# Optimization experiments

Hardware: AMD Instinct MI355X
Metric: run time of the kernel (lower is better)

## Reference

```python
import jax, jax.numpy as jnp
import numpy as np

# B=batch, T=time, H=hidden_size, D=vocos_dim, I=intermediate_dim, L=num_layers,
# CB=codebook_size, CD=codebook_dim (factorized VQ)
B, T, H, D, I, L, CB, CD = 8, 2048, 1024, 384, 2048, 12, 8192, 8


def _ln(h, g, b, eps=1e-6):
    # torch LayerNorm over last dim (biased variance)
    m = h.mean(-1, keepdims=True)
    v = h.var(-1, keepdims=True)
    return (h - m) / jnp.sqrt(v + eps) * g + b


def _conv1d(x, w, b, groups=1):
    # x: (B, Cin, T), w: (Cout, Cin//groups, 7), same-pad k=7
    y = jax.lax.conv_general_dilated(
        x, w, window_strides=(1,), padding=[(3, 3)],
        dimension_numbers=('NCH', 'OIH', 'NCH'), feature_group_count=groups)
    return y + b[None, :, None]


def setup_inputs() -> dict:
    key = jax.random.key(0)
    ks = iter(jax.random.split(key, 32))
    def nrm(shape):
        return jax.random.normal(next(ks), shape, jnp.float32) * 0.02
    d = {}
    d['x'] = jax.random.normal(next(ks), (B, T, H), jnp.float32)
    # VocosBackbone (encoder): embed conv + LN + 12 ConvNeXt blocks + final LN
    d['enc_embed_w'] = nrm((D, H, 7)); d['enc_embed_b'] = jnp.zeros((D,), jnp.float32)
    d['enc_norm_g'] = jnp.ones((D,), jnp.float32); d['enc_norm_b'] = jnp.zeros((D,), jnp.float32)
    d['enc_dw_w'] = nrm((L, D, 1, 7)); d['enc_dw_b'] = jnp.zeros((L, D), jnp.float32)
    d['enc_ln_g'] = jnp.ones((L, D), jnp.float32); d['enc_ln_b'] = jnp.zeros((L, D), jnp.float32)
    d['enc_w1'] = nrm((L, I, D)); d['enc_b1'] = jnp.zeros((L, I), jnp.float32)
    d['enc_w2'] = nrm((L, D, I)); d['enc_b2'] = jnp.zeros((L, D), jnp.float32)
    d['enc_gamma'] = jnp.full((L, D), 1.0 / L, jnp.float32)  # layer_scale init 1/num_layers
    d['enc_fnorm_g'] = jnp.ones((D,), jnp.float32); d['enc_fnorm_b'] = jnp.zeros((D,), jnp.float32)
    # nn.Linear(vocos_dim, hidden_size)
    d['enc_out_w'] = nrm((H, D)); d['enc_out_b'] = jnp.zeros((H,), jnp.float32)
    # Factorized ResidualVQ (single quantizer): 1024 -> 8, 8192-entry codebook, 8 -> 1024
    d['vq_in_w'] = nrm((CD, H)); d['vq_in_b'] = jnp.zeros((CD,), jnp.float32)
    d['codebook'] = jax.random.normal(next(ks), (CB, CD), jnp.float32)
    d['vq_out_w'] = nrm((H, CD)); d['vq_out_b'] = jnp.zeros((H,), jnp.float32)
    return d


def _encode(x, ew, eb, ng, nb, dww, dwb, lng, lnb, w1, b1, w2, b2, gamma, fg, fb, ow, ob):
    # x: (B, T, H) -> encoder output (B, T, H)
    h = _conv1d(x.transpose(0, 2, 1), ew, eb)            # (B, D, T)
    h = _ln(h.transpose(0, 2, 1), ng, nb)                # (B, T, D)
    for i in range(L):
        res = h
        y = _conv1d(h.transpose(0, 2, 1), dww[i], dwb[i], groups=D)  # depthwise (B, D, T)
        y = _ln(y.transpose(0, 2, 1), lng[i], lnb[i])                # (B, T, D)
        y = jax.nn.gelu(y @ w1[i].T + b1[i], approximate=False)       # (B, T, I)
        y = (y @ w2[i].T + b2[i]) * gamma[i]                          # (B, T, D)
        h = res + y
    h = _ln(h, fg, fb)
    return h @ ow.T + ob                                  # (B, T, H)


def _quantize(enc, in_w, in_b, codebook, out_w, out_b):
    z_e = enc @ in_w.T + in_b                             # (B, T, CD)
    z_n = z_e / jnp.maximum(jnp.linalg.norm(z_e, axis=-1, keepdims=True), 1e-12)
    cb_n = codebook / jnp.maximum(jnp.linalg.norm(codebook, axis=-1, keepdims=True), 1e-12)
    sim = jnp.einsum('btd,nd->btn', z_n, cb_n)            # cosine sim == argmin l2 on normalized vecs
    idx = jnp.argmax(sim, axis=-1)                        # (B, T) int
    z_q = codebook[idx]                                   # (B, T, CD) unnormalized codebook entries
    z_q = z_e + jax.lax.stop_gradient(z_q - z_e)          # straight-through estimator
    quantized = z_q @ out_w.T + out_b                     # (B, T, H)
    return idx, quantized


def reference(x, enc_embed_w, enc_embed_b, enc_norm_g, enc_norm_b, enc_dw_w, enc_dw_b,
              enc_ln_g, enc_ln_b, enc_w1, enc_b1, enc_w2, enc_b2, enc_gamma,
              enc_fnorm_g, enc_fnorm_b, enc_out_w, enc_out_b,
              vq_in_w, vq_in_b, codebook, vq_out_w, vq_out_b):
    enc = _encode(x, enc_embed_w, enc_embed_b, enc_norm_g, enc_norm_b, enc_dw_w, enc_dw_b,
                  enc_ln_g, enc_ln_b, enc_w1, enc_b1, enc_w2, enc_b2, enc_gamma,
                  enc_fnorm_g, enc_fnorm_b, enc_out_w, enc_out_b)
    idx, quantized = _quantize(enc, vq_in_w, vq_in_b, codebook, vq_out_w, vq_out_b)
    # RepCodec.quantize returns (indices (B,T), quantized_out.transpose(1,2) -> (B,T,H))
    return idx, quantized
```

## Files before the change

### kernel.cpp

```cpp
#include <hip/hip_runtime.h>
#include <math.h>


typedef _Float16 h8_t __attribute__((ext_vector_type(8)));
typedef _Float16 h4_t __attribute__((ext_vector_type(4)));
typedef float f4_t __attribute__((ext_vector_type(4)));

__device__ __forceinline__ float gelu_exact(float x){
  return 0.5f * x * (1.0f + erff(x * 0.70710678118654752f));
}

__device__ __forceinline__ void split8(const float4& a, const float4& b, h8_t& hi, h8_t& lo){
  float f[8] = {a.x,a.y,a.z,a.w,b.x,b.y,b.z,b.w};
  #pragma unroll
  for (int t=0;t<8;t++){
    _Float16 hh = (_Float16)f[t];
    hi[t] = hh;
    lo[t] = (_Float16)(f[t] - (float)hh);
  }
}

__device__ __forceinline__ void split4(const float4& a, h4_t& hi, h4_t& lo){
  float f[4] = {a.x,a.y,a.z,a.w};
  #pragma unroll
  for (int t=0;t<4;t++){
    _Float16 hh = (_Float16)f[t];
    hi[t] = hh;
    lo[t] = (_Float16)(f[t] - (float)hh);
  }
}

__device__ __forceinline__ int swz(int row, int kg){
  return row*32 + ((kg ^ ((row>>1)&3))<<3);
}

__device__ __forceinline__ void xcd_remap(int& bx, int& by){
  const int gx = gridDim.x;
  const int nwg = gx * gridDim.y;
  int bid = by*gx + bx;
  if ((nwg & 7) == 0){
    bid = (bid & 7)*(nwg >> 3) + (bid >> 3);
    bx = bid % gx; by = bid / gx;
  }
}


__global__ __launch_bounds__(256) void prep_wk_split(const float* __restrict__ w,
                                                     _Float16* __restrict__ wh,
                                                     _Float16* __restrict__ wl){
  int i = blockIdx.x*256 + threadIdx.x;
  if (i >= 384*1024) return;
  int d = i >> 10, c = i & 1023;
  #pragma unroll
  for (int k=0;k<7;k++){
    float v = w[(size_t)d*(1024*7) + (size_t)c*7 + k];
    _Float16 hh = (_Float16)v;
    wh[(size_t)k*393216 + i] = hh;
    wl[(size_t)k*393216 + i] = (_Float16)(v - (float)hh);
  }
}

__global__ __launch_bounds__(256) void prep_cb(const float* __restrict__ cb, float* __restrict__ cbn){
  int e = blockIdx.x*256 + threadIdx.x;
  if (e >= 8192) return;
  float v[8], s = 0.f;
  #pragma unroll
  for (int cd=0; cd<8; ++cd){ v[cd] = cb[(size_t)e*8+cd]; s += v[cd]*v[cd]; }
  float inv = 1.0f / fmaxf(sqrtf(s), 1e-12f);
  #pragma unroll
  for (int cd=0; cd<8; ++cd) cbn[(size_t)e*8+cd] = v[cd]*inv;
}

__global__ __launch_bounds__(256) void split_pair(const float* __restrict__ a, const float* __restrict__ b,
                                                  _Float16* __restrict__ ah, _Float16* __restrict__ al,
                                                  _Float16* __restrict__ bh, _Float16* __restrict__ bl,
                                                  int n4){
  int i = blockIdx.x*256 + threadIdx.x;
  if (i >= n4) return;
  h4_t hi, lo;
  float4 va = ((const float4*)a)[i];
  split4(va, hi, lo);
  ((h4_t*)ah)[i] = hi; ((h4_t*)al)[i] = lo;
  float4 vb = ((const float4*)b)[i];
  split4(vb, hi, lo);
  ((h4_t*)bh)[i] = hi; ((h4_t*)bl)[i] = lo;
}

__global__ __launch_bounds__(256) void split_one(const float* __restrict__ a,
                                                 _Float16* __restrict__ ah, _Float16* __restrict__ al,
                                                 int n4){
  int i = blockIdx.x*256 + threadIdx.x;
  if (i >= n4) return;
  h4_t hi, lo;
  float4 va = ((const float4*)a)[i];
  split4(va, hi, lo);
  ((h4_t*)ah)[i] = hi; ((h4_t*)al)[i] = lo;
}

template<int BN, int EPI>
__global__ __launch_bounds__(256,2) void gemm_s(
    const _Float16* __restrict__ Ah, const _Float16* __restrict__ Al, int lda,
    const _Float16* __restrict__ Bh, const _Float16* __restrict__ Bl, int ldb,
    const float* __restrict__ bias, const float* __restrict__ gamma,
    float* __restrict__ C, _Float16* __restrict__ Ch, _Float16* __restrict__ Cl,
    int ldc, int K)
{
  constexpr int NF = BN/32;
  __shared__ _Float16 AsH[4096], AsL[4096];
  __shared__ _Float16 BsH[BN*32], BsL[BN*32];
  const int tid = threadIdx.x;
  int bx = blockIdx.x, by = blockIdx.y;
  xcd_remap(bx, by);
  const int m0 = by*128, n0 = bx*BN;
  const int srow = tid>>2, kgs = tid&3, koff = kgs*8;
  const _Float16* pAh = Ah + (size_t)(m0+srow)*lda + koff;
  const _Float16* pAl = Al + (size_t)(m0+srow)*lda + koff;
  const _Float16* pBh = Bh + (size_t)(n0+srow)*ldb + koff;
  const _Float16* pBl = Bl + (size_t)(n0+srow)*ldb + koff;
  const int sA0 = swz(srow, kgs), sA1 = swz(srow+64, kgs);
  const int lane = tid & 63, wid = tid >> 6;
  const int wm = (wid>>1)*64, wn = (wid&1)*(BN/2);
  const int fr = lane & 15, kg = lane >> 4;
  f4_t acc[4][NF] = {};
  h8_t rah0 = *(const h8_t*)(pAh);
  h8_t rah1 = *(const h8_t*)(pAh + (size_t)64*lda);
  h8_t ral0 = *(const h8_t*)(pAl);
  h8_t ral1 = *(const h8_t*)(pAl + (size_t)64*lda);
  h8_t rbh0 = *(const h8_t*)(pBh);
  h8_t rbl0 = *(const h8_t*)(pBl);
  h8_t rbh1, rbl1;
  if constexpr (BN == 128){
    rbh1 = *(const h8_t*)(pBh + (size_t)64*ldb);
    rbl1 = *(const h8_t*)(pBl + (size_t)64*ldb);
  }
  for (int k0 = 0; k0 < K; k0 += 32){
    __syncthreads();
    *(h8_t*)(AsH + sA0) = rah0; *(h8_t*)(AsL + sA0) = ral0;
    *(h8_t*)(AsH + sA1) = rah1; *(h8_t*)(AsL + sA1) = ral1;
    *(h8_t*)(BsH + sA0) = rbh0; *(h8_t*)(BsL + sA0) = rbl0;
    if constexpr (BN == 128){
      *(h8_t*)(BsH + sA1) = rbh1; *(h8_t*)(BsL + sA1) = rbl1;
    }
    if (k0 + 32 < K){
      const int kn = k0 + 32;
      rah0 = *(const h8_t*)(pAh + kn);
      rah1 = *(const h8_t*)(pAh + (size_t)64*lda + kn);
      ral0 = *(const h8_t*)(pAl + kn);
      ral1 = *(const h8_t*)(pAl + (size_t)64*lda + kn);
      rbh0 = *(const h8_t*)(pBh + kn);
      rbl0 = *(const h8_t*)(pBl + kn);
      if constexpr (BN == 128){
        rbh1 = *(const h8_t*)(pBh + (size_t)64*ldb + kn);
        rbl1 = *(const h8_t*)(pBl + (size_t)64*ldb + kn);
      }
    }
    __syncthreads();
    h8_t ah[4], al[4], bh[NF], bl[NF];
    #pragma unroll
    for (int m=0;m<4;m++){
      int o = swz(wm + fr + m*16, kg);
      ah[m] = *(const h8_t*)(AsH + o);
      al[m] = *(const h8_t*)(AsL + o);
    }
    #pragma unroll
    for (int n=0;n<NF;n++){
      int o = swz(wn + fr + n*16, kg);
      bh[n] = *(const h8_t*)(BsH + o);
      bl[n] = *(const h8_t*)(BsL + o);
    }
    #pragma unroll
    for (int m=0;m<4;m++)
      #pragma unroll
      for (int n=0;n<NF;n++){
        acc[m][n] = __builtin_amdgcn_mfma_f32_16x16x32_f16(al[m], bh[n], acc[m][n], 0,0,0);
        acc[m][n] = __builtin_amdgcn_mfma_f32_16x16x32_f16(ah[m], bl[n], acc[m][n], 0,0,0);
        acc[m][n] = __builtin_amdgcn_mfma_f32_16x16x32_f16(ah[m], bh[n], acc[m][n], 0,0,0);
      }
  }
  float bj[NF], gj[NF];
  #pragma unroll
  for (int n=0;n<NF;n++){
    int col = n0 + wn + n*16 + fr;
    bj[n] = bias ? bias[col] : 0.0f;
    gj[n] = (EPI==2) ? gamma[col] : 0.0f;
  }
  #pragma unroll
  for (int m=0;m<4;m++){
    #pragma unroll
    for (int r=0;r<4;r++){
      const int row = m0 + wm + m*16 + kg*4 + r;
      #pragma unroll
      for (int n=0;n<NF;n++){
        const int col = n0 + wn + n*16 + fr;
        float v = acc[m][n][r] + bj[n];
        if (EPI==0){
          C[(size_t)row*ldc + col] = v;
        } else if (EPI==1){
          v = gelu_exact(v);
          _Float16 hh = (_Float16)v;
          Ch[(size_t)row*ldc + col] = hh;
          Cl[(size_t)row*ldc + col] = (_Float16)(v - (float)hh);
        } else if (EPI==2){
          C[(size_t)row*ldc + col] += gj[n]*v;
        } else {
          _Float16 hh = (_Float16)v;
          Ch[(size_t)row*ldc + col] = hh;
          Cl[(size_t)row*ldc + col] = (_Float16)(v - (float)hh);
        }
      }
    }
  }
}

__global__ __launch_bounds__(256,2) void embed_f16(
    const float* __restrict__ x, const _Float16* __restrict__ wkh, const _Float16* __restrict__ wkl,
    const float* __restrict__ bias, float* __restrict__ C)
{
  __shared__ _Float16 AsH[4096], AsL[4096], BsH[2048], BsL[2048];
  const int tid = threadIdx.x;
  int bx = blockIdx.x, by = blockIdx.y;
  xcd_remap(bx, by);
  const int m0 = by*128, n0 = bx*64;
  const int srow = tid>>2, kgs = tid&3, koff = kgs*8;
  const int sA0 = swz(srow, kgs), sA1 = swz(srow+64, kgs);
  const int lane = tid & 63, wid = tid >> 6;
  const int wm = (wid>>1)*64, wn = (wid&1)*32;
  const int fr = lane & 15, kg = lane >> 4;
  const int r0 = m0 + srow, r1 = r0 + 64;
  const int t0 = r0 & 2047, t1 = r1 & 2047;
  f4_t acc[4][2] = {};
  for (int k=0;k<7;k++){
    const bool v0 = (unsigned)(t0 + k - 3) < 2048u;
    const bool v1 = (unsigned)(t1 + k - 3) < 2048u;
    const float* xp0 = x + (size_t)(r0 + k - 3)*1024 + koff;
    const float* xp1 = x + (size_t)(r1 + k - 3)*1024 + koff;
    const _Float16* wph = wkh + (size_t)k*393216 + (size_t)(n0+srow)*1024 + koff;
    const _Float16* wpl = wkl + (size_t)k*393216 + (size_t)(n0+srow)*1024 + koff;
    for (int k0=0;k0<1024;k0+=32){
      float4 a0a = make_float4(0,0,0,0), a0b = a0a, a1a = a0a, a1b = a0a;
      if (v0){ a0a = *(const float4*)(xp0+k0); a0b = *(const float4*)(xp0+k0+4); }
      if (v1){ a1a = *(const float4*)(xp1+k0); a1b = *(const float4*)(xp1+k0+4); }
      h8_t bvh = *(const h8_t*)(wph + k0);
      h8_t bvl = *(const h8_t*)(wpl + k0);
      __syncthreads();
      h8_t hi, lo;
      split8(a0a,a0b,hi,lo); *(h8_t*)(AsH+sA0)=hi; *(h8_t*)(AsL+sA0)=lo;
      split8(a1a,a1b,hi,lo); *(h8_t*)(AsH+sA1)=hi; *(h8_t*)(AsL+sA1)=lo;
      *(h8_t*)(BsH+sA0)=bvh; *(h8_t*)(BsL+sA0)=bvl;
      __syncthreads();
      h8_t ah[4], al[4], bh[2], bl[2];
      #pragma unroll
      for (int m=0;m<4;m++){
        int o = swz(wm + fr + m*16, kg);
        ah[m] = *(const h8_t*)(AsH + o);
        al[m] = *(const h8_t*)(AsL + o);
      }
      #pragma unroll
      for (int n=0;n<2;n++){
        int o = swz(wn + fr + n*16, kg);
        bh[n] = *(const h8_t*)(BsH + o);
        bl[n] = *(const h8_t*)(BsL + o);
      }
      #pragma unroll
      for (int m=0;m<4;m++)
        #pragma unroll
        for (int n=0;n<2;n++){
          acc[m][n] = __builtin_amdgcn_mfma_f32_16x16x32_f16(al[m], bh[n], acc[m][n], 0,0,0);
          acc[m][n] = __builtin_amdgcn_mfma_f32_16x16x32_f16(ah[m], bl[n], acc[m][n], 0,0,0);
          acc[m][n] = __builtin_amdgcn_mfma_f32_16x16x32_f16(ah[m], bh[n], acc[m][n], 0,0,0);
        }
    }
  }
  #pragma unroll
  for (int m=0;m<4;m++){
    #pragma unroll
    for (int r=0;r<4;r++){
      const int row = m0 + wm + m*16 + kg*4 + r;
      #pragma unroll
      for (int n=0;n<2;n++){
        const int col = n0 + wn + n*16 + fr;
        C[(size_t)row*384 + col] = acc[m][n][r] + bias[col];
      }
    }
  }
}

template<bool CONV, bool SPLIT>
__global__ __launch_bounds__(384) void ln_kernel(
    const float* __restrict__ in,
    const float* __restrict__ dw, const float* __restrict__ db,
    const float* __restrict__ g, const float* __restrict__ b,
    float* __restrict__ out, _Float16* __restrict__ oh, _Float16* __restrict__ ol)
{
  __shared__ float rs[6], rs2[6], stat[2];
  const int m = blockIdx.x, d = threadIdx.x;
  float v;
  if (CONV){
    const int t = m & 2047;
    float a = db[d];
    #pragma unroll
    for (int k=0;k<7;k++){
      int tt = t + k - 3;
      if ((unsigned)tt < 2048u) a = fmaf(in[(size_t)(m + k - 3)*384 + d], dw[d*7 + k], a);
    }
    v = a;
  } else {
    v = in[(size_t)m*384 + d];
  }
  float s = v, s2 = v*v;
  #pragma unroll
  for (int o=1;o<64;o<<=1){ s += __shfl_xor(s,o); s2 += __shfl_xor(s2,o); }
  const int wid = d >> 6, lane = d & 63;
  if (lane == 0){ rs[wid]=s; rs2[wid]=s2; }
  __syncthreads();
  if (d == 0){
    float S=0.f, S2=0.f;
    #pragma unroll
    for (int w=0;w<6;w++){ S+=rs[w]; S2+=rs2[w]; }
    float mean = S*(1.0f/384.0f);
    float var = fmaxf(S2*(1.0f/384.0f) - mean*mean, 0.0f);
    stat[0]=mean; stat[1]=1.0f/sqrtf(var + 1e-6f);
  }
  __syncthreads();
  float o = (v - stat[0])*stat[1]*g[d] + b[d];
  if (SPLIT){
    _Float16 hh = (_Float16)o;
    oh[(size_t)m*384 + d] = hh;
    ol[(size_t)m*384 + d] = (_Float16)(o - (float)hh);
  } else {
    out[(size_t)m*384 + d] = o;
  }
}


__global__ __launch_bounds__(256) void vq_in_kernel(
    const _Float16* __restrict__ ench, const _Float16* __restrict__ encl,
    const float* __restrict__ wi, const float* __restrict__ bi, float* __restrict__ zn)
{
  __shared__ float sw[8192];
  const int tid = threadIdx.x;
  for (int i = tid*4; i < 8192; i += 1024) *(float4*)&sw[i] = *(const float4*)&wi[i];
  __syncthreads();
  const int wid = tid >> 6, lane = tid & 63;
  const size_t m = (size_t)blockIdx.x*4 + wid;
  float acc[8] = {};
  for (int j=0;j<16;j++){
    float v = (float)ench[m*1024 + j*64 + lane] + (float)encl[m*1024 + j*64 + lane];
    #pragma unroll
    for (int cd=0;cd<8;cd++) acc[cd] = fmaf(v, sw[cd*1024 + j*64 + lane], acc[cd]);
  }
  #pragma unroll
  for (int cd=0;cd<8;cd++)
    #pragma unroll
    for (int o=1;o<64;o<<=1) acc[cd] += __shfl_xor(acc[cd], o);
  if (lane == 0){
    float z[8], s = 0.f;
    #pragma unroll
    for (int cd=0;cd<8;cd++){ z[cd] = acc[cd] + bi[cd]; s += z[cd]*z[cd]; }
    float inv = 1.0f / fmaxf(sqrtf(s), 1e-12f);
    #pragma unroll
    for (int cd=0;cd<8;cd++) zn[m*8+cd] = z[cd]*inv;
  }
}

__global__ __launch_bounds__(256) void vq_argmax(
    const float* __restrict__ zn, const float* __restrict__ cbn,
    int* __restrict__ idx_out, float* __restrict__ idx_f)
{
  __shared__ float sbest[256];
  __shared__ int   sidx[256];
  const int tid = threadIdx.x;
  const int tok = tid & 31, ch = tid >> 5;
  const size_t m = (size_t)blockIdx.x*32 + tok;
  float4 z0 = *(const float4*)&zn[m*8];
  float4 z1 = *(const float4*)&zn[m*8+4];
  float best = -1e30f; int bidx = 0;
  const float* cp = cbn + (size_t)ch*8192;
  #pragma unroll 4
  for (int e = 0; e < 1024; ++e){
    const float4 ca  = *(const float4*)&cp[e*8];
    const float4 cb4 = *(const float4*)&cp[e*8+4];
    float s = z0.x*ca.x + z0.y*ca.y + z0.z*ca.z + z0.w*ca.w
            + z1.x*cb4.x + z1.y*cb4.y + z1.z*cb4.z + z1.w*cb4.w;
    if (s > best){ best = s; bidx = ch*1024 + e; }
  }
  sbest[tid] = best; sidx[tid] = bidx;
  __syncthreads();
  if (tid < 32){
    float b = sbest[tid]; int bi = sidx[tid];
    #pragma unroll
    for (int c=1;c<8;c++){
      float ob = sbest[c*32 + tid];
      if (ob > b){ b = ob; bi = sidx[c*32 + tid]; }
    }
    idx_out[(size_t)blockIdx.x*32 + tid] = bi;
    idx_f [(size_t)blockIdx.x*32 + tid] = (float)bi;
  }
}

__global__ __launch_bounds__(256) void vq_out_kernel(
    const int* __restrict__ idx, const float* __restrict__ cb,
    const float* __restrict__ wo, const float* __restrict__ bo,
    float* __restrict__ outq)
{
  __shared__ float wT[8][1024];
  __shared__ float cbs[16][8];
  __shared__ int idxs[16];
  const int tid = threadIdx.x;
  #pragma unroll
  for (int j=0;j<4;j++){
    int hcol = j*256 + tid;
    float4 w0 = *(const float4*)&wo[(size_t)hcol*8];
    float4 w1 = *(const float4*)&wo[(size_t)hcol*8+4];
    wT[0][hcol]=w0.x; wT[1][hcol]=w0.y; wT[2][hcol]=w0.z; wT[3][hcol]=w0.w;
    wT[4][hcol]=w1.x; wT[5][hcol]=w1.y; wT[6][hcol]=w1.z; wT[7][hcol]=w1.w;
  }
  if (tid < 16) idxs[tid] = idx[blockIdx.x*16 + tid];
  __syncthreads();
  if (tid < 128){ int tk = tid>>3, cd = tid&7; cbs[tk][cd] = cb[(size_t)idxs[tk]*8 + cd]; }
  __syncthreads();
  float bb[4];
  #pragma unroll
  for (int j=0;j<4;j++) bb[j] = bo[j*256+tid];
  for (int tk=0;tk<16;tk++){
    const size_t m = (size_t)blockIdx.x*16 + tk;
    float c0=cbs[tk][0], c1=cbs[tk][1], c2=cbs[tk][2], c3=cbs[tk][3];
    float c4=cbs[tk][4], c5=cbs[tk][5], c6=cbs[tk][6], c7=cbs[tk][7];
    #pragma unroll
    for (int j=0;j<4;j++){
      int hcol = j*256 + tid;
      float v = bb[j];
      v = fmaf(c0, wT[0][hcol], v); v = fmaf(c1, wT[1][hcol], v);
      v = fmaf(c2, wT[2][hcol], v); v = fmaf(c3, wT[3][hcol], v);
      v = fmaf(c4, wT[4][hcol], v); v = fmaf(c5, wT[5][hcol], v);
      v = fmaf(c6, wT[6][hcol], v); v = fmaf(c7, wT[7][hcol], v);
      outq[m*1024 + hcol] = v;
    }
  }
}


extern "C" void kernel_launch(void* const* d_in, const int* in_sizes, int n_in,
                              void* d_out, int out_size, void* d_ws, size_t ws_size,
                              hipStream_t stream) {
  (void)in_sizes; (void)n_in; (void)out_size; (void)ws_size;
  const float* x   = (const float*)d_in[0];
  const float* eww = (const float*)d_in[1];
  const float* ewb = (const float*)d_in[2];
  const float* ng  = (const float*)d_in[3];
  const float* nb  = (const float*)d_in[4];
  const float* dww = (const float*)d_in[5];
  const float* dwb = (const float*)d_in[6];
  const float* lng = (const float*)d_in[7];
  const float* lnb = (const float*)d_in[8];
  const float* w1  = (const float*)d_in[9];
  const float* b1  = (const float*)d_in[10];
  const float* w2  = (const float*)d_in[11];
  const float* b2  = (const float*)d_in[12];
  const float* gma = (const float*)d_in[13];
  const float* fg  = (const float*)d_in[14];
  const float* fb  = (const float*)d_in[15];
  const float* ow  = (const float*)d_in[16];
  const float* ob  = (const float*)d_in[17];
  const float* viw = (const float*)d_in[18];
  const float* vib = (const float*)d_in[19];
  const float* cb  = (const float*)d_in[20];
  const float* vow = (const float*)d_in[21];
  const float* vob = (const float*)d_in[22];
  float* out = (float*)d_out;

  float* ws = (float*)d_ws;
  float* wreg = ws;
  _Float16* wkh = (_Float16*)wreg;
  _Float16* wkl = wkh + 2752512;
  _Float16* w1h = (_Float16*)wreg;
  _Float16* w1l = w1h + 786432;
  _Float16* w2h = w1h + 1572864;
  _Float16* w2l = w1h + 2359296;
  _Float16* owh = (_Float16*)wreg;
  _Float16* owl = owh + 393216;
  float* zn  = wreg + 1048576;
  float* cbn = wreg + 1179648;
  int*  idxb = (int*)(wreg + 1245184);
  float* h   = ws + 2752512;
  _Float16* ylh = (_Float16*)(ws + 9043968);
  _Float16* yll = ylh + 6291456;
  float* y1reg = ws + 15335424;
  float* yf32 = y1reg;
  _Float16* y1h = (_Float16*)y1reg;
  _Float16* y1l = y1h + 16777216;
  _Float16* ench = y1h;
  _Float16* encl = y1l;

  prep_wk_split<<<dim3(1536), dim3(256), 0, stream>>>(eww, wkh, wkl);
  embed_f16<<<dim3(6,128), dim3(256), 0, stream>>>(x, wkh, wkl, ewb, yf32);
  ln_kernel<false,false><<<dim3(16384), dim3(384), 0, stream>>>(
      yf32, nullptr, nullptr, ng, nb, h, nullptr, nullptr);

  for (int i = 0; i < 12; ++i){
    split_pair<<<dim3(768), dim3(256), 0, stream>>>(
        w1 + (size_t)i*786432, w2 + (size_t)i*786432, w1h, w1l, w2h, w2l, 196608);
    ln_kernel<true,true><<<dim3(16384), dim3(384), 0, stream>>>(
        h, dww + (size_t)i*2688, dwb + (size_t)i*384,
        lng + (size_t)i*384, lnb + (size_t)i*384, nullptr, ylh, yll);
    for (int ic = 0; ic < 2; ++ic){
      gemm_s<128,1><<<dim3(8,128), dim3(256), 0, stream>>>(
          ylh, yll, 384,
          w1h + (size_t)ic*393216, w1l + (size_t)ic*393216, 384,
          b1 + (size_t)i*2048 + (size_t)ic*1024, nullptr,
          nullptr, y1h, y1l, 1024, 384);
      gemm_s<64,2><<<dim3(6,128), dim3(256), 0, stream>>>(
          y1h, y1l, 1024,
          w2h + (size_t)ic*1024, w2l + (size_t)ic*1024, 2048,
          (ic == 0) ? (b2 + (size_t)i*384) : nullptr,
          gma + (size_t)i*384,
          h, nullptr, nullptr, 384, 1024);
    }
  }

  ln_kernel<false,true><<<dim3(16384), dim3(384), 0, stream>>>(
      h, nullptr, nullptr, fg, fb, nullptr, ylh, yll);
  split_one<<<dim3(384), dim3(256), 0, stream>>>(ow, owh, owl, 98304);
  gemm_s<128,3><<<dim3(8,128), dim3(256), 0, stream>>>(
      ylh, yll, 384, owh, owl, 384, ob, nullptr,
      nullptr, ench, encl, 1024, 384);

  prep_cb<<<dim3(32), dim3(256), 0, stream>>>(cb, cbn);
  vq_in_kernel<<<dim3(4096), dim3(256), 0, stream>>>(ench, encl, viw, vib, zn);
  vq_argmax<<<dim3(512), dim3(256), 0, stream>>>(zn, cbn, idxb, out);
  vq_out_kernel<<<dim3(1024), dim3(256), 0, stream>>>(idxb, cb, vow, vob, out + 16384);
}
```

Measured before the change: 3.752 ms.

## Double-buffer GEMM LDS tiles, pre-split embed input, fold enc_out into VQ projection

The GEMM and embed-conv kernels now use double-buffered shared-memory tiles with a single barrier per k-step and raised wave priority around the MFMA block. This overlaps global loads and LDS writes with matrix math. The embed input is split into fp16 hi/lo once by a separate kernel, so the conv-GEMM no longer converts it inside its loop. The encoder output linear (1024x384) is folded algebraically into the 8-dim VQ input projection, which removes a large GEMM and its 1024-wide intermediate, at the cost of a small weight-product prep kernel and a different fp32 rounding order.

```diff
diff --git a/kernel.cpp b/kernel.cpp
--- a/kernel.cpp
+++ b/kernel.cpp
@@ -8,16 +8,6 @@
 
 __device__ __forceinline__ float gelu_exact(float x){
   return 0.5f * x * (1.0f + erff(x * 0.70710678118654752f));
-}
-
-__device__ __forceinline__ void split8(const float4& a, const float4& b, h8_t& hi, h8_t& lo){
-  float f[8] = {a.x,a.y,a.z,a.w,b.x,b.y,b.z,b.w};
-  #pragma unroll
-  for (int t=0;t<8;t++){
-    _Float16 hh = (_Float16)f[t];
-    hi[t] = hh;
-    lo[t] = (_Float16)(f[t] - (float)hh);
-  }
 }
 
 __device__ __forceinline__ void split4(const float4& a, h4_t& hi, h4_t& lo){
@@ -69,6 +59,25 @@
   float inv = 1.0f / fmaxf(sqrtf(s), 1e-12f);
   #pragma unroll
   for (int cd=0; cd<8; ++cd) cbn[(size_t)e*8+cd] = v[cd]*inv;
+}
+
+__global__ __launch_bounds__(256) void prep_cw(const float* __restrict__ viw, const float* __restrict__ ow,
+                                               const float* __restrict__ vib, const float* __restrict__ ob,
+                                               float* __restrict__ cw, float* __restrict__ cbias){
+  int i = blockIdx.x*256 + threadIdx.x;
+  if (i < 3072){
+    int c = i / 384, d = i - c*384;
+    float acc = 0.f;
+    for (int h=0; h<1024; ++h)
+      acc = fmaf(viw[c*1024+h], ow[(size_t)h*384 + d], acc);
+    cw[i] = acc;
+  }
+  if (blockIdx.x == 0 && threadIdx.x < 8){
+    int c = threadIdx.x;
+    float acc = vib[c];
+    for (int h=0; h<1024; ++h) acc = fmaf(viw[c*1024+h], ob[h], acc);
+    cbias[c] = acc;
+  }
 }
 
 __global__ __launch_bounds__(256) void split_pair(const float* __restrict__ a, const float* __restrict__ b,
@@ -106,8 +115,9 @@
     int ldc, int K)
 {
   constexpr int NF = BN/32;
-  __shared__ _Float16 AsH[4096], AsL[4096];
-  __shared__ _Float16 BsH[BN*32], BsL[BN*32];
+  constexpr int ASZ = 4096, BSZ = BN*32;
+  __shared__ _Float16 AsH[2*ASZ], AsL[2*ASZ];
+  __shared__ _Float16 BsH[2*BSZ], BsL[2*BSZ];
   const int tid = threadIdx.x;
   int bx = blockIdx.x, by = blockIdx.y;
   xcd_remap(bx, by);
@@ -122,52 +132,55 @@
   const int wm = (wid>>1)*64, wn = (wid&1)*(BN/2);
   const int fr = lane & 15, kg = lane >> 4;
   f4_t acc[4][NF] = {};
-  h8_t rah0 = *(const h8_t*)(pAh);
-  h8_t rah1 = *(const h8_t*)(pAh + (size_t)64*lda);
-  h8_t ral0 = *(const h8_t*)(pAl);
-  h8_t ral1 = *(const h8_t*)(pAl + (size_t)64*lda);
-  h8_t rbh0 = *(const h8_t*)(pBh);
-  h8_t rbl0 = *(const h8_t*)(pBl);
-  h8_t rbh1, rbl1;
-  if constexpr (BN == 128){
-    rbh1 = *(const h8_t*)(pBh + (size_t)64*ldb);
-    rbl1 = *(const h8_t*)(pBl + (size_t)64*ldb);
-  }
-  for (int k0 = 0; k0 < K; k0 += 32){
-    __syncthreads();
-    *(h8_t*)(AsH + sA0) = rah0; *(h8_t*)(AsL + sA0) = ral0;
-    *(h8_t*)(AsH + sA1) = rah1; *(h8_t*)(AsL + sA1) = ral1;
-    *(h8_t*)(BsH + sA0) = rbh0; *(h8_t*)(BsL + sA0) = rbl0;
+  const int nt = K >> 5;
+  h8_t rah0, rah1, ral0, ral1, rbh0, rbl0, rbh1, rbl1;
+  auto gload = [&](int t){
+    const int kn = t << 5;
+    rah0 = *(const h8_t*)(pAh + kn);
+    rah1 = *(const h8_t*)(pAh + (size_t)64*lda + kn);
+    ral0 = *(const h8_t*)(pAl + kn);
+    ral1 = *(const h8_t*)(pAl + (size_t)64*lda + kn);
+    rbh0 = *(const h8_t*)(pBh + kn);
+    rbl0 = *(const h8_t*)(pBl + kn);
     if constexpr (BN == 128){
-      *(h8_t*)(BsH + sA1) = rbh1; *(h8_t*)(BsL + sA1) = rbl1;
-    }
-    if (k0 + 32 < K){
-      const int kn = k0 + 32;
-      rah0 = *(const h8_t*)(pAh + kn);
-      rah1 = *(const h8_t*)(pAh + (size_t)64*lda + kn);
-      ral0 = *(const h8_t*)(pAl + kn);
-      ral1 = *(const h8_t*)(pAl + (size_t)64*lda + kn);
-      rbh0 = *(const h8_t*)(pBh + kn);
-      rbl0 = *(const h8_t*)(pBl + kn);
-      if constexpr (BN == 128){
-        rbh1 = *(const h8_t*)(pBh + (size_t)64*ldb + kn);
-        rbl1 = *(const h8_t*)(pBl + (size_t)64*ldb + kn);
-      }
-    }
-    __syncthreads();
+      rbh1 = *(const h8_t*)(pBh + (size_t)64*ldb + kn);
+      rbl1 = *(const h8_t*)(pBl + (size_t)64*ldb + kn);
+    }
+  };
+  auto swrite = [&](int b){
+    _Float16* aH = AsH + b*ASZ; _Float16* aL = AsL + b*ASZ;
+    _Float16* bH = BsH + b*BSZ; _Float16* bL = BsL + b*BSZ;
+    *(h8_t*)(aH + sA0) = rah0; *(h8_t*)(aL + sA0) = ral0;
+    *(h8_t*)(aH + sA1) = rah1; *(h8_t*)(aL + sA1) = ral1;
+    *(h8_t*)(bH + sA0) = rbh0; *(h8_t*)(bL + sA0) = rbl0;
+    if constexpr (BN == 128){
+      *(h8_t*)(bH + sA1) = rbh1; *(h8_t*)(bL + sA1) = rbl1;
+    }
+  };
+  gload(0);
+  swrite(0);
+  if (nt > 1) gload(1);
+  __syncthreads();
+  int cur = 0;
+  for (int t = 0; t < nt; ++t){
+    const _Float16* aH = AsH + cur*ASZ; const _Float16* aL = AsL + cur*ASZ;
+    const _Float16* bH = BsH + cur*BSZ; const _Float16* bL = BsL + cur*BSZ;
     h8_t ah[4], al[4], bh[NF], bl[NF];
     #pragma unroll
     for (int m=0;m<4;m++){
       int o = swz(wm + fr + m*16, kg);
-      ah[m] = *(const h8_t*)(AsH + o);
-      al[m] = *(const h8_t*)(AsL + o);
+      ah[m] = *(const h8_t*)(aH + o);
+      al[m] = *(const h8_t*)(aL + o);
     }
     #pragma unroll
     for (int n=0;n<NF;n++){
       int o = swz(wn + fr + n*16, kg);
-      bh[n] = *(const h8_t*)(BsH + o);
-      bl[n] = *(const h8_t*)(BsL + o);
-    }
+      bh[n] = *(const h8_t*)(bH + o);
+      bl[n] = *(const h8_t*)(bL + o);
+    }
+    if (t + 1 < nt) swrite(cur^1);
+    if (t + 2 < nt) gload(t + 2);
+    __builtin_amdgcn_s_setprio(1);
     #pragma unroll
     for (int m=0;m<4;m++)
       #pragma unroll
@@ -176,6 +189,9 @@
         acc[m][n] = __builtin_amdgcn_mfma_f32_16x16x32_f16(ah[m], bl[n], acc[m][n], 0,0,0);
         acc[m][n] = __builtin_amdgcn_mfma_f32_16x16x32_f16(ah[m], bh[n], acc[m][n], 0,0,0);
       }
+    __builtin_amdgcn_s_setprio(0);
+    __syncthreads();
+    cur ^= 1;
   }
   float bj[NF], gj[NF];
   #pragma unroll
@@ -213,10 +229,12 @@
 }
 
 __global__ __launch_bounds__(256,2) void embed_f16(
-    const float* __restrict__ x, const _Float16* __restrict__ wkh, const _Float16* __restrict__ wkl,
+    const _Float16* __restrict__ xh, const _Float16* __restrict__ xl,
+    const _Float16* __restrict__ wkh, const _Float16* __restrict__ wkl,
     const float* __restrict__ bias, float* __restrict__ C)
 {
-  __shared__ _Float16 AsH[4096], AsL[4096], BsH[2048], BsL[2048];
+  constexpr int ASZ = 4096, BSZ = 2048;
+  __shared__ _Float16 AsH[2*ASZ], AsL[2*ASZ], BsH[2*BSZ], BsL[2*BSZ];
   const int tid = threadIdx.x;
   int bx = blockIdx.x, by = blockIdx.y;
   xcd_remap(bx, by);
@@ -229,47 +247,65 @@
   const int r0 = m0 + srow, r1 = r0 + 64;
   const int t0 = r0 & 2047, t1 = r1 & 2047;
   f4_t acc[4][2] = {};
-  for (int k=0;k<7;k++){
+  const h8_t zero8 = {0,0,0,0,0,0,0,0};
+  h8_t rah0, rah1, ral0, ral1, rbh0, rbl0;
+  auto load_tile = [&](int kt){
+    const int k = kt >> 5;
+    const int k0 = (kt & 31) << 5;
     const bool v0 = (unsigned)(t0 + k - 3) < 2048u;
     const bool v1 = (unsigned)(t1 + k - 3) < 2048u;
-    const float* xp0 = x + (size_t)(r0 + k - 3)*1024 + koff;
-    const float* xp1 = x + (size_t)(r1 + k - 3)*1024 + koff;
-    const _Float16* wph = wkh + (size_t)k*393216 + (size_t)(n0+srow)*1024 + koff;
-    const _Float16* wpl = wkl + (size_t)k*393216 + (size_t)(n0+srow)*1024 + koff;
-    for (int k0=0;k0<1024;k0+=32){
-      float4 a0a = make_float4(0,0,0,0), a0b = a0a, a1a = a0a, a1b = a0a;
-      if (v0){ a0a = *(const float4*)(xp0+k0); a0b = *(const float4*)(xp0+k0+4); }
-      if (v1){ a1a = *(const float4*)(xp1+k0); a1b = *(const float4*)(xp1+k0+4); }
-      h8_t bvh = *(const h8_t*)(wph + k0);
-      h8_t bvl = *(const h8_t*)(wpl + k0);
-      __syncthreads();
-      h8_t hi, lo;
-      split8(a0a,a0b,hi,lo); *(h8_t*)(AsH+sA0)=hi; *(h8_t*)(AsL+sA0)=lo;
-      split8(a1a,a1b,hi,lo); *(h8_t*)(AsH+sA1)=hi; *(h8_t*)(AsL+sA1)=lo;
-      *(h8_t*)(BsH+sA0)=bvh; *(h8_t*)(BsL+sA0)=bvl;
-      __syncthreads();
-      h8_t ah[4], al[4], bh[2], bl[2];
-      #pragma unroll
-      for (int m=0;m<4;m++){
-        int o = swz(wm + fr + m*16, kg);
-        ah[m] = *(const h8_t*)(AsH + o);
-        al[m] = *(const h8_t*)(AsL + o);
-      }
+    rah0 = zero8; rah1 = zero8; ral0 = zero8; ral1 = zero8;
+    if (v0){
+      const size_t o = (size_t)(r0 + k - 3)*1024 + k0 + koff;
+      rah0 = *(const h8_t*)(xh + o); ral0 = *(const h8_t*)(xl + o);
+    }
+    if (v1){
+      const size_t o = (size_t)(r1 + k - 3)*1024 + k0 + koff;
+      rah1 = *(const h8_t*)(xh + o); ral1 = *(const h8_t*)(xl + o);
+    }
+    const size_t wo = (size_t)k*393216 + (size_t)(n0+srow)*1024 + k0 + koff;
+    rbh0 = *(const h8_t*)(wkh + wo); rbl0 = *(const h8_t*)(wkl + wo);
+  };
+  auto swrite = [&](int b){
+    *(h8_t*)(AsH + b*ASZ + sA0) = rah0; *(h8_t*)(AsL + b*ASZ + sA0) = ral0;
+    *(h8_t*)(AsH + b*ASZ + sA1) = rah1; *(h8_t*)(AsL + b*ASZ + sA1) = ral1;
+    *(h8_t*)(BsH + b*BSZ + sA0) = rbh0; *(h8_t*)(BsL + b*BSZ + sA0) = rbl0;
+  };
+  load_tile(0);
+  swrite(0);
+  load_tile(1);
+  __syncthreads();
+  int cur = 0;
+  for (int kt = 0; kt < 224; ++kt){
+    const _Float16* aH = AsH + cur*ASZ; const _Float16* aL = AsL + cur*ASZ;
+    const _Float16* bH = BsH + cur*BSZ; const _Float16* bL = BsL + cur*BSZ;
+    h8_t ah[4], al[4], bh[2], bl[2];
+    #pragma unroll
+    for (int m=0;m<4;m++){
+      int o = swz(wm + fr + m*16, kg);
+      ah[m] = *(const h8_t*)(aH + o);
+      al[m] = *(const h8_t*)(aL + o);
+    }
+    #pragma unroll
+    for (int n=0;n<2;n++){
+      int o = swz(wn + fr + n*16, kg);
+      bh[n] = *(const h8_t*)(bH + o);
+      bl[n] = *(const h8_t*)(bL + o);
+    }
+    if (kt + 1 < 224) swrite(cur^1);
+    if (kt + 2 < 224) load_tile(kt + 2);
+    __builtin_amdgcn_s_setprio(1);
+    #pragma unroll
+    for (int m=0;m<4;m++)
       #pragma unroll
       for (int n=0;n<2;n++){
-        int o = swz(wn + fr + n*16, kg);
-        bh[n] = *(const h8_t*)(BsH + o);
-        bl[n] = *(const h8_t*)(BsL + o);
+        acc[m][n] = __builtin_amdgcn_mfma_f32_16x16x32_f16(al[m], bh[n], acc[m][n], 0,0,0);
+        acc[m][n] = __builtin_amdgcn_mfma_f32_16x16x32_f16(ah[m], bl[n], acc[m][n], 0,0,0);
+        acc[m][n] = __builtin_amdgcn_mfma_f32_16x16x32_f16(ah[m], bh[n], acc[m][n], 0,0,0);
       }
-      #pragma unroll
-      for (int m=0;m<4;m++)
-        #pragma unroll
-        for (int n=0;n<2;n++){
-          acc[m][n] = __builtin_amdgcn_mfma_f32_16x16x32_f16(al[m], bh[n], acc[m][n], 0,0,0);
-          acc[m][n] = __builtin_amdgcn_mfma_f32_16x16x32_f16(ah[m], bl[n], acc[m][n], 0,0,0);
-          acc[m][n] = __builtin_amdgcn_mfma_f32_16x16x32_f16(ah[m], bh[n], acc[m][n], 0,0,0);
-        }
-    }
+    __builtin_amdgcn_s_setprio(0);
+    __syncthreads();
+    cur ^= 1;
   }
   #pragma unroll
   for (int m=0;m<4;m++){
@@ -333,21 +369,22 @@
 }
 
 
-__global__ __launch_bounds__(256) void vq_in_kernel(
-    const _Float16* __restrict__ ench, const _Float16* __restrict__ encl,
-    const float* __restrict__ wi, const float* __restrict__ bi, float* __restrict__ zn)
+__global__ __launch_bounds__(256) void vq_ze(
+    const float* __restrict__ y, const float* __restrict__ cw,
+    const float* __restrict__ cbias, float* __restrict__ zn)
 {
-  __shared__ float sw[8192];
+  __shared__ float scw[3072];
   const int tid = threadIdx.x;
-  for (int i = tid*4; i < 8192; i += 1024) *(float4*)&sw[i] = *(const float4*)&wi[i];
+  for (int i = tid; i < 3072; i += 256) scw[i] = cw[i];
   __syncthreads();
   const int wid = tid >> 6, lane = tid & 63;
   const size_t m = (size_t)blockIdx.x*4 + wid;
   float acc[8] = {};
-  for (int j=0;j<16;j++){
-    float v = (float)ench[m*1024 + j*64 + lane] + (float)encl[m*1024 + j*64 + lane];
-    #pragma unroll
-    for (int cd=0;cd<8;cd++) acc[cd] = fmaf(v, sw[cd*1024 + j*64 + lane], acc[cd]);
+  #pragma unroll
+  for (int j=0;j<6;j++){
+    float v = y[m*384 + j*64 + lane];
+    #pragma unroll
+    for (int cd=0;cd<8;cd++) acc[cd] = fmaf(v, scw[cd*384 + j*64 + lane], acc[cd]);
   }
   #pragma unroll
   for (int cd=0;cd<8;cd++)
@@ -356,7 +393,7 @@
   if (lane == 0){
     float z[8], s = 0.f;
     #pragma unroll
-    for (int cd=0;cd<8;cd++){ z[cd] = acc[cd] + bi[cd]; s += z[cd]*z[cd]; }
+    for (int cd=0;cd<8;cd++){ z[cd] = acc[cd] + cbias[cd]; s += z[cd]*z[cd]; }
     float inv = 1.0f / fmaxf(sqrtf(s), 1e-12f);
     #pragma unroll
     for (int cd=0;cd<8;cd++) zn[m*8+cd] = z[cd]*inv;
@@ -477,23 +514,25 @@
   _Float16* w1l = w1h + 786432;
   _Float16* w2h = w1h + 1572864;
   _Float16* w2l = w1h + 2359296;
-  _Float16* owh = (_Float16*)wreg;
-  _Float16* owl = owh + 393216;
   float* zn  = wreg + 1048576;
   float* cbn = wreg + 1179648;
   int*  idxb = (int*)(wreg + 1245184);
+  float* cw  = wreg + 1261568;
+  float* cbias = wreg + 1264640;
   float* h   = ws + 2752512;
-  _Float16* ylh = (_Float16*)(ws + 9043968);
+  float* ylreg = ws + 9043968;
+  float* yf32 = ylreg;
+  _Float16* ylh = (_Float16*)ylreg;
   _Float16* yll = ylh + 6291456;
   float* y1reg = ws + 15335424;
-  float* yf32 = y1reg;
+  _Float16* xh  = (_Float16*)y1reg;
+  _Float16* xl  = xh + 16777216;
   _Float16* y1h = (_Float16*)y1reg;
   _Float16* y1l = y1h + 16777216;
-  _Float16* ench = y1h;
-  _Float16* encl = y1l;
 
   prep_wk_split<<<dim3(1536), dim3(256), 0, stream>>>(eww, wkh, wkl);
-  embed_f16<<<dim3(6,128), dim3(256), 0, stream>>>(x, wkh, wkl, ewb, yf32);
+  split_one<<<dim3(16384), dim3(256), 0, stream>>>(x, xh, xl, 4194304);
+  embed_f16<<<dim3(6,128), dim3(256), 0, stream>>>(xh, xl, wkh, wkl, ewb, yf32);
   ln_kernel<false,false><<<dim3(16384), dim3(384), 0, stream>>>(
       yf32, nullptr, nullptr, ng, nb, h, nullptr, nullptr);
 
@@ -518,15 +557,11 @@
     }
   }
 
-  ln_kernel<false,true><<<dim3(16384), dim3(384), 0, stream>>>(
-      h, nullptr, nullptr, fg, fb, nullptr, ylh, yll);
-  split_one<<<dim3(384), dim3(256), 0, stream>>>(ow, owh, owl, 98304);
-  gemm_s<128,3><<<dim3(8,128), dim3(256), 0, stream>>>(
-      ylh, yll, 384, owh, owl, 384, ob, nullptr,
-      nullptr, ench, encl, 1024, 384);
-
+  ln_kernel<false,false><<<dim3(16384), dim3(384), 0, stream>>>(
+      h, nullptr, nullptr, fg, fb, yf32, nullptr, nullptr);
+  prep_cw<<<dim3(12), dim3(256), 0, stream>>>(viw, ow, vib, ob, cw, cbias);
   prep_cb<<<dim3(32), dim3(256), 0, stream>>>(cb, cbn);
-  vq_in_kernel<<<dim3(4096), dim3(256), 0, stream>>>(ench, encl, viw, vib, zn);
+  vq_ze<<<dim3(4096), dim3(256), 0, stream>>>(yf32, cw, cbias, zn);
   vq_argmax<<<dim3(512), dim3(256), 0, stream>>>(zn, cbn, idxb, out);
   vq_out_kernel<<<dim3(1024), dim3(256), 0, stream>>>(idxb, cb, vow, vob, out + 16384);
 }
```

Result: no change. 3.810 ms (+1.5%).
